# Kernel optimization log

Hardware: AMD Instinct MI355X
Metric: run time of the kernel (lower is better)

## Reference

```python
import jax, jax.numpy as jnp
import numpy as np

B, N, D = 1, 40962, 512
H, HD = 4, 128            # num_heads, key_size=value_size=d_model//num_heads
BS = 256                  # mask_block_size
NB = 161                  # num blocks = ceil(N/BS)
NP = NB * BS              # padded nodes = 41216
PAD = NP - N              # num_padding_nodes = 254
C = 16                    # global_norm_conditioning dim
FFW = 4 * D
SCALE = HD ** -0.5


def _build_mask():
    valid = (np.arange(NP) < N).reshape(NB, BS)            # key validity per block
    md = np.broadcast_to(valid[:, None, :], (NB, BS, BS))  # diag: keys of block n
    mu = np.zeros((NB, BS, BS), bool)
    mu[:-1] = np.broadcast_to(valid[1:, None, :], (NB - 1, BS, BS))   # upper: block n+1
    ml = np.zeros((NB, BS, BS), bool)
    ml[1:] = np.broadcast_to(valid[:-1, None, :], (NB - 1, BS, BS))   # lower: block n-1
    m = np.stack([md, mu, ml])[None, :, :, None]           # [1,3,NB,1,BS,BS]
    return jnp.asarray(m)


def setup_inputs() -> dict:
    key = jax.random.key(0)
    ks = jax.random.split(key, 12)
    s = 0.02
    return {
        'x': jax.random.normal(ks[0], (B, N, D), jnp.float32),
        'global_norm_conditioning': jax.random.normal(ks[1], (B, C), jnp.float32),
        'mask': _build_mask(),
        'wq': jax.random.normal(ks[2], (D, H * HD), jnp.float32) * s,
        'wk': jax.random.normal(ks[3], (D, H * HD), jnp.float32) * s,
        'wv': jax.random.normal(ks[4], (D, H * HD), jnp.float32) * s,
        'w_final': jax.random.normal(ks[5], (H * HD, D), jnp.float32) * s,
        'b_final': jnp.zeros((D,), jnp.float32),
        'w_up': jax.random.normal(ks[6], (D, FFW), jnp.float32) * s,
        'b_up': jnp.zeros((FFW,), jnp.float32),
        'w_down': jax.random.normal(ks[7], (FFW, D), jnp.float32) * s,
        'b_down': jnp.zeros((D,), jnp.float32),
        'w_cond': jax.random.normal(ks[8], (C, 2 * D), jnp.float32) * s,
        'b_cond': jnp.zeros((2 * D,), jnp.float32),
    }


def _layernorm(h):
    mu = h.mean(-1, keepdims=True)
    var = h.var(-1, keepdims=True)
    return (h - mu) * jax.lax.rsqrt(var + 1e-5)


def _triblock_attn(h, mask, wq, wk, wv, w_final, b_final):
    hp = jnp.pad(h, ((0, 0), (0, PAD), (0, 0))).reshape(B, NB, BS, D)
    q = (hp @ wq).reshape(B, NB, BS, H, HD)
    k = (hp @ wk).reshape(B, NB, BS, H, HD)
    v = (hp @ wv).reshape(B, NB, BS, H, HD)
    k = jnp.pad(k, ((0, 0), (1, 1), (0, 0), (0, 0), (0, 0)))
    v = jnp.pad(v, ((0, 0), (1, 1), (0, 0), (0, 0), (0, 0)))
    qk = lambda kk: jnp.einsum('bnqhd,bnkhd->bnhqk', q, kk) * SCALE
    ld = jnp.where(mask[:, 0], qk(k[:, 1:-1]), -1e30)
    lu = jnp.where(mask[:, 1], qk(k[:, 2:]), -1e30)
    ll = jnp.where(mask[:, 2], qk(k[:, :-2]), -1e30)
    # tri-block softmax with shared max/denominator
    m = jnp.maximum(jnp.maximum(
        jax.lax.stop_gradient(ld.max(-1, keepdims=True)),
        jax.lax.stop_gradient(lu.max(-1, keepdims=True))),
        jax.lax.stop_gradient(ll.max(-1, keepdims=True)))
    ed, eu, el = jnp.exp(ld - m), jnp.exp(lu - m), jnp.exp(ll - m)
    denom = ed.sum(-1, keepdims=True) + eu.sum(-1, keepdims=True) + el.sum(-1, keepdims=True)
    av = lambda w, vv: jnp.einsum('bnhqk,bnkhd->bnqhd', w, vv)
    o = av(ed / denom, v[:, 1:-1]) + av(eu / denom, v[:, 2:]) + av(el / denom, v[:, :-2])
    o = o.reshape(B, NP, H * HD) @ w_final + b_final
    return o[:, :N, :]


def reference(x, global_norm_conditioning, mask, wq, wk, wv, w_final, b_final,
              w_up, b_up, w_down, b_down, w_cond, b_cond):
    so = global_norm_conditioning @ w_cond + b_cond       # [B, 2D]
    scale, offset = jnp.split(so[:, None, :], 2, axis=-1)  # [B,1,D] each
    cond = lambda h: h * (scale + 1.0) + offset
    x = x + _triblock_attn(cond(_layernorm(x)), mask, wq, wk, wv, w_final, b_final)
    h = cond(_layernorm(x))
    x = x + (jax.nn.gelu(h @ w_up + b_up) @ w_down + b_down)
    return x
```

## Files before the change

### kernel.cpp

```cpp
#include <hip/hip_runtime.h>
#include <stdint.h>
#include <stddef.h>

#define NNODES 40962
#define NBLK   161
#define NP     41216
#define DM     512
#define NH     4
#define HD     128
#define SCALE_ATT 0.08838834764831845f

typedef __attribute__((ext_vector_type(8))) short short8;
typedef __attribute__((ext_vector_type(4))) float f32x4;
typedef __attribute__((ext_vector_type(4))) unsigned short us4;
typedef __attribute__((ext_vector_type(8))) __bf16 bf16x8;

__device__ __forceinline__ unsigned short f2bf(float f){
  unsigned u = __builtin_bit_cast(unsigned, f);
  u += 0x7fffu + ((u >> 16) & 1u);
  return (unsigned short)(u >> 16);
}
__device__ __forceinline__ float bf2f(unsigned short h){
  unsigned u = ((unsigned)h) << 16;
  return __builtin_bit_cast(float, u);
}
__device__ __forceinline__ unsigned char f2fp8(float f){
  return (unsigned char)(__builtin_amdgcn_cvt_pk_fp8_f32(f, 0.f, 0, false) & 0xff);
}
__device__ __forceinline__ float gelu_tanh(float x){
  float y = 0.7978845608028654f * (x + 0.044715f * x * x * x);
  y = fminf(fmaxf(y, -15.f), 15.f);
  float t = __expf(2.f * y);
  return x * t / (t + 1.f);
}
__device__ __forceinline__ bf16x8 ldb8(const unsigned short* p){
  return *(const bf16x8*)p;
}
#define MFMA(a,b,c) __builtin_amdgcn_mfma_f32_16x16x32_bf16((a),(b),(c),0,0,0)
#define MFMA8(a,b,c) __builtin_amdgcn_mfma_f32_16x16x32_fp8_fp8((a),(b),(c),0,0,0)

#define GLOAD16(g, l) \
  __builtin_amdgcn_global_load_lds((const __attribute__((address_space(1))) unsigned int*)(g), \
                                   (__attribute__((address_space(3))) unsigned int*)(l), 16, 0, 0)

__global__ void k_cond(const float* __restrict__ gnc, const float* __restrict__ wc,
                       const float* __restrict__ bc, float* __restrict__ cond){
  int j = blockIdx.x * 256 + threadIdx.x;
  float acc = bc[j];
  #pragma unroll
  for(int c = 0; c < 16; ++c) acc += gnc[c] * wc[c * 1024 + j];
  cond[j] = (j < 512) ? acc + 1.0f : acc;
}

__global__ __launch_bounds__(256) void k_transpose_f8(const float* __restrict__ W,
                                                      unsigned char* __restrict__ Wt,
                                                      int K, int Ncols){
  __shared__ float tile[32][33];
  int n0 = blockIdx.x * 32, k0 = blockIdx.y * 32;
  int tx = threadIdx.x & 31, ty = threadIdx.x >> 5;
  #pragma unroll
  for(int i = 0; i < 4; ++i){
    int r = ty + i * 8;
    tile[r][tx] = W[(size_t)(k0 + r) * Ncols + n0 + tx];
  }
  __syncthreads();
  #pragma unroll
  for(int i = 0; i < 4; ++i){
    int r = ty + i * 8;
    Wt[(size_t)(n0 + r) * K + k0 + tx] = f2fp8(tile[tx][r]);
  }
}

__global__ __launch_bounds__(256) void k_lncond(const void* __restrict__ xin, int in_bf16,
                                                const float* __restrict__ cond,
                                                void* __restrict__ outv, int out_f8,
                                                int Mvalid){
  int lane = threadIdx.x & 63;
  int row = blockIdx.x * 4 + (threadIdx.x >> 6);
  if(row >= Mvalid){
    if(out_f8){
      unsigned char* orow = (unsigned char*)outv + (size_t)row * DM + lane * 8;
      *(uint2*)orow = make_uint2(0, 0);
    } else {
      unsigned short* orow = (unsigned short*)outv + (size_t)row * DM + lane * 8;
      *(uint4*)orow = make_uint4(0,0,0,0);
    }
    return;
  }
  float v[8];
  if(in_bf16){
    const unsigned short* xr = (const unsigned short*)xin + (size_t)row * DM + lane * 8;
    us4 a = *(const us4*)xr, b = *(const us4*)(xr + 4);
    #pragma unroll
    for(int j = 0; j < 4; ++j){ v[j] = bf2f(a[j]); v[4+j] = bf2f(b[j]); }
  } else {
    const float* xr = (const float*)xin + (size_t)row * DM + lane * 8;
    float4 a = *(const float4*)xr;
    float4 b = *(const float4*)(xr + 4);
    v[0]=a.x; v[1]=a.y; v[2]=a.z; v[3]=a.w; v[4]=b.x; v[5]=b.y; v[6]=b.z; v[7]=b.w;
  }
  float s = 0.f, s2 = 0.f;
  #pragma unroll
  for(int j = 0; j < 8; ++j){ s += v[j]; s2 += v[j]*v[j]; }
  #pragma unroll
  for(int off = 1; off < 64; off <<= 1){ s += __shfl_xor(s, off); s2 += __shfl_xor(s2, off); }
  float mu = s * (1.f/DM);
  float var = s2 * (1.f/DM) - mu*mu;
  float rs = rsqrtf(var + 1e-5f);
  float scv[8], ofv[8];
  {
    float4 sc0 = *(const float4*)(cond + lane*8);
    float4 sc1 = *(const float4*)(cond + lane*8 + 4);
    float4 of0 = *(const float4*)(cond + 512 + lane*8);
    float4 of1 = *(const float4*)(cond + 512 + lane*8 + 4);
    scv[0]=sc0.x;scv[1]=sc0.y;scv[2]=sc0.z;scv[3]=sc0.w;
    scv[4]=sc1.x;scv[5]=sc1.y;scv[6]=sc1.z;scv[7]=sc1.w;
    ofv[0]=of0.x;ofv[1]=of0.y;ofv[2]=of0.z;ofv[3]=of0.w;
    ofv[4]=of1.x;ofv[5]=of1.y;ofv[6]=of1.z;ofv[7]=of1.w;
  }
  float o8[8];
  #pragma unroll
  for(int j = 0; j < 8; ++j) o8[j] = (v[j] - mu) * rs * scv[j] + ofv[j];
  if(out_f8){
    unsigned char* orow = (unsigned char*)outv + (size_t)row * DM + lane * 8;
    unsigned lo = 0, hi = 0;
    #pragma unroll
    for(int j = 0; j < 4; ++j) lo |= ((unsigned)f2fp8(o8[j])) << (8*j);
    #pragma unroll
    for(int j = 0; j < 4; ++j) hi |= ((unsigned)f2fp8(o8[4+j])) << (8*j);
    *(uint2*)orow = make_uint2(lo, hi);
  } else {
    unsigned short* orow = (unsigned short*)outv + (size_t)row * DM + lane * 8;
    unsigned pk[4];
    #pragma unroll
    for(int j = 0; j < 4; ++j)
      pk[j] = (unsigned)f2bf(o8[2*j]) | ((unsigned)f2bf(o8[2*j+1]) << 16);
    *(uint4*)orow = make_uint4(pk[0],pk[1],pk[2],pk[3]);
  }
}

#define GF_GELU   1
#define GF_RESF32 4
#define GF_QKV    8
#define GF_F8OUT  16

__global__ __launch_bounds__(256, 3)
void k_g128_f8(const unsigned char* __restrict__ A, int lda,
               const unsigned char* __restrict__ Bt, int ldb,
               const float* __restrict__ bias,
               const void* __restrict__ resid, int ldr,
               void* __restrict__ out, int ldo,
               void* __restrict__ out_k, void* __restrict__ out_vt,
               int Mstore, int NT, int Nblks, int flags)
{
  __shared__ __align__(16) unsigned char As[128*128];
  __shared__ __align__(16) unsigned char Bs[128*128];
  const int tid = threadIdx.x;
  const int lane = tid & 63, l15 = lane & 15, lg = lane >> 4;
  const int w = tid >> 6, wm = w >> 1, wn = w & 1;
  int nwg = gridDim.x;
  int q = nwg >> 3, r = nwg & 7;
  int xcd = blockIdx.x & 7, idx = blockIdx.x >> 3;
  int sid = (xcd < r ? xcd * (q + 1) : r * (q + 1) + (xcd - r) * q) + idx;
  int mblk = sid / Nblks, nblk = sid % Nblks;
  const int m0 = mblk * 128, n0 = nblk * 128;

  int srow[4], scol[4];
  #pragma unroll
  for(int rr = 0; rr < 4; ++rr){
    unsigned L = (unsigned)rr * 4096u + (unsigned)tid * 16u;
    unsigned sw = L ^ (((L >> 7) & 7u) << 4);
    srow[rr] = sw >> 7;
    scol[rr] = sw & 127u;
  }
  const unsigned wbase = (unsigned)w * 1024u;

  f32x4 acc[4][4];
  #pragma unroll
  for(int i = 0; i < 4; ++i)
    #pragma unroll
    for(int j = 0; j < 4; ++j) acc[i][j] = (f32x4)0.0f;

  for(int ks = 0; ks < NT; ++ks){
    #pragma unroll
    for(int rr = 0; rr < 4; ++rr)
      GLOAD16(A + (size_t)(m0 + srow[rr]) * lda + ks*128 + scol[rr],
              (char*)As + rr*4096 + wbase);
    #pragma unroll
    for(int rr = 0; rr < 4; ++rr)
      GLOAD16(Bt + (size_t)(n0 + srow[rr]) * ldb + ks*128 + scol[rr],
              (char*)Bs + rr*4096 + wbase);
    __syncthreads();
    #pragma unroll
    for(int kk = 0; kk < 4; ++kk){
      const unsigned csw = (unsigned)((kk*32 + lg*8) ^ ((l15 & 7) << 4));
      long la[4], lb[4];
      #pragma unroll
      for(int mi = 0; mi < 4; ++mi)
        la[mi] = *(const long*)(As + (wm*64 + mi*16 + l15)*128 + csw);
      #pragma unroll
      for(int ni = 0; ni < 4; ++ni)
        lb[ni] = *(const long*)(Bs + (wn*64 + ni*16 + l15)*128 + csw);
      #pragma unroll
      for(int mi = 0; mi < 4; ++mi)
        #pragma unroll
        for(int ni = 0; ni < 4; ++ni)
          acc[mi][ni] = MFMA8(la[mi], lb[ni], acc[mi][ni]);
    }
    __syncthreads();
  }

  unsigned short* bdst = (unsigned short*)out;
  int cadj = 0;
  bool vtrans = false;
  bool qscale = false;
  if(flags & GF_QKV){
    if(n0 < 512)       { bdst = (unsigned short*)out;    cadj = 0; qscale = true; }
    else if(n0 < 1024) { bdst = (unsigned short*)out_k;  cadj = 512; }
    else               { bdst = (unsigned short*)out_vt; cadj = 1024; vtrans = true; }
  }
  #pragma unroll
  for(int mi = 0; mi < 4; ++mi){
    int rowb = m0 + wm*64 + mi*16 + lg*4;
    #pragma unroll
    for(int ni = 0; ni < 4; ++ni){
      int col = n0 + wn*64 + ni*16 + l15;
      float bc = bias ? bias[col] : 0.f;
      float vv[4];
      #pragma unroll
      for(int rr = 0; rr < 4; ++rr){
        float tt = acc[mi][ni][rr] + bc;
        if(flags & GF_GELU) tt = gelu_tanh(tt);
        if(qscale) tt *= SCALE_ATT;
        vv[rr] = tt;
      }
      if(flags & GF_QKV){
        if(vtrans){
          us4 pk;
          #pragma unroll
          for(int rr = 0; rr < 4; ++rr) pk[rr] = f2bf(vv[rr]);
          *(us4*)(bdst + (size_t)(col - cadj)*NP + rowb) = pk;
        } else {
          #pragma unroll
          for(int rr = 0; rr < 4; ++rr)
            bdst[(size_t)(rowb + rr)*ldo + col - cadj] = f2bf(vv[rr]);
        }
      } else if(flags & GF_F8OUT){
        #pragma unroll
        for(int rr = 0; rr < 4; ++rr)
          ((unsigned char*)out)[(size_t)(rowb + rr)*ldo + col] = f2fp8(vv[rr]);
      } else if(flags & GF_RESF32){
        #pragma unroll
        for(int rr = 0; rr < 4; ++rr){
          int row = rowb + rr;
          if(row < Mstore){
            float tt = vv[rr] + ((const float*)resid)[(size_t)row*ldr + col];
            ((unsigned short*)out)[(size_t)row*ldo + col] = f2bf(tt);
          }
        }
      } else {
        #pragma unroll
        for(int rr = 0; rr < 4; ++rr){
          int row = rowb + rr;
          if(row < Mstore){
            float tt = vv[rr]
                     + bf2f(((const unsigned short*)resid)[(size_t)row*ldr + col]);
            ((float*)out)[(size_t)row*ldo + col] = tt;
          }
        }
      }
    }
  }
}

__global__ __launch_bounds__(512, 4)
void k_attn(const unsigned short* __restrict__ q_g, const unsigned short* __restrict__ k_g,
            const unsigned short* __restrict__ vt_g, unsigned char* __restrict__ o_g8)
{
  __shared__ __align__(16) unsigned short kv[128*128];
  __shared__ __align__(16) unsigned short p_lds[8*16*136];
  int b = blockIdx.x;
  int g = (b & 7) * 161 + (b >> 3);
  int n = g >> 3, rg = (g >> 2) & 1, h = g & 3;
  int tid = threadIdx.x;
  int w = tid >> 6, lane = tid & 63, l15 = lane & 15, lg = lane >> 4;
  int qbase = n*256 + rg*128 + w*16;
  unsigned short* pw = p_lds + w*16*136;
  const int rsw = (l15 & 7) << 3;
  const int srow = tid >> 4, scs = (tid & 15) * 8;

  bf16x8 aq[4];
  {
    const unsigned short* qp = q_g + (size_t)(qbase + l15)*DM + h*HD + lg*8;
    #pragma unroll
    for(int kb = 0; kb < 4; ++kb) aq[kb] = ldb8(qp + kb*32);
  }
  f32x4 oacc[8];
  #pragma unroll
  for(int t = 0; t < 8; ++t) oacc[t] = (f32x4)0.0f;
  float denom[4] = {0.f,0.f,0.f,0.f};

  #define COORDS(j, K0, VCH) do {                                    \
    int d_ = (j) >> 1, ch_ = (j) & 1;                                \
    int nb_ = n + (d_ == 1 ? 1 : (d_ == 2 ? -1 : 0));                \
    int nbc_ = nb_ < 0 ? 0 : (nb_ >= NBLK ? NBLK - 1 : nb_);         \
    (K0) = nbc_*256 + ch_*128;                                       \
    (VCH) = (nb_ >= 0) && (nb_ < NBLK) && ((K0) < NNODES);           \
  } while(0)

  short8 kreg[4], vreg[4];
  int k0; bool vch;
  COORDS(0, k0, vch);
  #pragma unroll
  for(int i = 0; i < 4; ++i){
    int row = srow + i*32;
    kreg[i] = *(const short8*)(k_g + (size_t)(k0+row)*DM + h*HD + scs);
    vreg[i] = *(const short8*)(vt_g + (size_t)(h*HD+row)*NP + k0 + scs);
  }

  #pragma unroll 1
  for(int j = 0; j < 6; ++j){
    int k0n = 0; bool vchn = false;
    const bool hn = (j < 5);
    if(hn) COORDS(j+1, k0n, vchn);
    __syncthreads();
    #pragma unroll
    for(int i = 0; i < 4; ++i){
      int row = srow + i*32;
      *(short8*)(kv + row*128 + (scs ^ ((row & 7) << 3))) = kreg[i];
    }
    __syncthreads();
    if(hn){
      #pragma unroll
      for(int i = 0; i < 4; ++i){
        int row = srow + i*32;
        kreg[i] = *(const short8*)(k_g + (size_t)(k0n+row)*DM + h*HD + scs);
      }
    }
    float rsum[4] = {0.f,0.f,0.f,0.f};
    #pragma unroll
    for(int t = 0; t < 8; ++t){
      f32x4 s = (f32x4)0.0f;
      #pragma unroll
      for(int kb = 0; kb < 4; ++kb){
        bf16x8 bk = ldb8(kv + (t*16 + l15)*128 + ((kb*32 + lg*8) ^ rsw));
        s = MFMA(aq[kb], bk, s);
      }
      bool kval = vch && ((k0 + t*16 + l15) < NNODES);
      #pragma unroll
      for(int r = 0; r < 4; ++r){
        float p = kval ? __expf(s[r]) : 0.f;
        rsum[r] += p;
        pw[(lg*4 + r)*136 + t*16 + l15] = f2bf(p);
      }
    }
    #pragma unroll
    for(int r = 0; r < 4; ++r){
      float s_ = rsum[r];
      s_ += __shfl_xor(s_, 1); s_ += __shfl_xor(s_, 2);
      s_ += __shfl_xor(s_, 4); s_ += __shfl_xor(s_, 8);
      denom[r] += s_;
    }
    __syncthreads();
    #pragma unroll
    for(int i = 0; i < 4; ++i){
      int row = srow + i*32;
      *(short8*)(kv + row*128 + (scs ^ ((row & 7) << 3))) = vreg[i];
    }
    __syncthreads();
    if(hn){
      #pragma unroll
      for(int i = 0; i < 4; ++i){
        int row = srow + i*32;
        vreg[i] = *(const short8*)(vt_g + (size_t)(h*HD+row)*NP + k0n + scs);
      }
    }
    __builtin_amdgcn_s_setprio(1);
    #pragma unroll
    for(int kb2 = 0; kb2 < 4; ++kb2){
      bf16x8 ap = ldb8(pw + l15*136 + kb2*32 + lg*8);
      #pragma unroll
      for(int t2 = 0; t2 < 8; ++t2){
        bf16x8 bv = ldb8(kv + (t2*16 + l15)*128 + ((kb2*32 + lg*8) ^ rsw));
        oacc[t2] = MFMA(ap, bv, oacc[t2]);
      }
    }
    __builtin_amdgcn_s_setprio(0);
    k0 = k0n; vch = vchn;
  }
  float inv[4];
  #pragma unroll
  for(int r = 0; r < 4; ++r) inv[r] = 1.0f / denom[r];
  #pragma unroll
  for(int t2 = 0; t2 < 8; ++t2){
    #pragma unroll
    for(int r = 0; r < 4; ++r){
      o_g8[(size_t)(qbase + lg*4 + r)*DM + h*HD + t2*16 + l15] =
        f2fp8(oacc[t2][r] * inv[r]);
    }
  }
}

extern "C" void kernel_launch(void* const* d_in, const int* in_sizes, int n_in,
                              void* d_out, int out_size, void* d_ws, size_t ws_size,
                              hipStream_t stream)
{
  const float* x    = (const float*)d_in[0];
  const float* gnc  = (const float*)d_in[1];
  const float* wq   = (const float*)d_in[3];
  const float* wk   = (const float*)d_in[4];
  const float* wv   = (const float*)d_in[5];
  const float* wf   = (const float*)d_in[6];
  const float* bfin = (const float*)d_in[7];
  const float* wup  = (const float*)d_in[8];
  const float* bup  = (const float*)d_in[9];
  const float* wdn  = (const float*)d_in[10];
  const float* bdn  = (const float*)d_in[11];
  const float* wc   = (const float*)d_in[12];
  const float* bc   = (const float*)d_in[13];
  float* out = (float*)d_out;

  char* ws = (char*)d_ws;
  size_t off = 0;
  auto alloc = [&](size_t bytes)->void*{
    void* p = ws + off;
    off += (bytes + 255) & ~(size_t)255;
    return p;
  };
  float*          cond    = (float*)alloc(1024u*4);
  unsigned char*  wqkv_f8 = (unsigned char*)alloc((size_t)1536*512);
  unsigned char*  wf_f8   = (unsigned char*)alloc((size_t)512*512);
  unsigned char*  wup_f8  = (unsigned char*)alloc((size_t)2048*512);
  unsigned char*  wdn_f8  = (unsigned char*)alloc((size_t)512*2048);
  unsigned char*  hp8     = (unsigned char*)alloc((size_t)NP*DM);
  unsigned short* kbuf    = (unsigned short*)alloc((size_t)NP*DM*2);
  unsigned short* vtbuf   = (unsigned short*)alloc((size_t)NP*DM*2);
  unsigned short* qbuf    = (unsigned short*)alloc((size_t)NP*DM*2);
  unsigned char*  obuf8   = (unsigned char*)alloc((size_t)NP*DM);
  unsigned short* x1      = (unsigned short*)alloc((size_t)NP*DM*2);
  unsigned char*  ubuf8   = (unsigned char*)alloc((size_t)NP*2048);
  (void)ws_size; (void)in_sizes; (void)n_in; (void)out_size;

  k_cond<<<4, 256, 0, stream>>>(gnc, wc, bc, cond);
  k_transpose_f8<<<dim3(16,16), 256, 0, stream>>>(wq, wqkv_f8,            512, 512);
  k_transpose_f8<<<dim3(16,16), 256, 0, stream>>>(wk, wqkv_f8 + 512*512,  512, 512);
  k_transpose_f8<<<dim3(16,16), 256, 0, stream>>>(wv, wqkv_f8 + 1024*512, 512, 512);
  k_transpose_f8<<<dim3(16,16), 256, 0, stream>>>(wf, wf_f8,  512, 512);
  k_transpose_f8<<<dim3(64,16), 256, 0, stream>>>(wup, wup_f8, 512, 2048);
  k_transpose_f8<<<dim3(16,64), 256, 0, stream>>>(wdn, wdn_f8, 2048, 512);
  k_lncond<<<NP/4, 256, 0, stream>>>(x, 0, cond, hp8, 1, NNODES);
  k_g128_f8<<<322*12, 256, 0, stream>>>(hp8, 512, wqkv_f8, 512, nullptr, nullptr, 0,
                                        qbuf, 512, kbuf, vtbuf, NP, 4, 12, GF_QKV);
  k_attn<<<1288, 512, 0, stream>>>(qbuf, kbuf, vtbuf, obuf8);
  k_g128_f8<<<322*4, 256, 0, stream>>>(obuf8, 512, wf_f8, 512, bfin, x, 512,
                                       x1, 512, nullptr, nullptr, NNODES, 4, 4,
                                       GF_RESF32);
  k_lncond<<<NP/4, 256, 0, stream>>>(x1, 1, cond, hp8, 1, NNODES);
  k_g128_f8<<<322*16, 256, 0, stream>>>(hp8, 512, wup_f8, 512, bup, nullptr, 0,
                                        ubuf8, 2048, nullptr, nullptr, NP, 4, 16,
                                        GF_GELU | GF_F8OUT);
  k_g128_f8<<<322*4, 256, 0, stream>>>(ubuf8, 2048, wdn_f8, 2048, bdn, x1, 512,
                                       out, 512, nullptr, nullptr, NNODES, 16, 4, 0);
}
```

Baseline: 557.1 us.

## Store Q/K/V in FP8 and run attention MFMAs in FP8

The QKV GEMM epilogue now writes Q, K and transposed V as FP8 bytes instead of bf16. The attention kernel loads FP8 operands and uses 16x16x32 fp8 MFMAs for both QK^T and PV, quantizing the probabilities to FP8 as well. The softmax scale moves from the Q store to the exp argument. This halves Q/K/V memory traffic and LDS footprint, at the cost of reduced accuracy in the scores and the probability-weighted sums.

```diff
diff --git a/kernel.cpp b/kernel.cpp
--- a/kernel.cpp
+++ b/kernel.cpp
@@ -13,6 +13,7 @@
 typedef __attribute__((ext_vector_type(8))) short short8;
 typedef __attribute__((ext_vector_type(4))) float f32x4;
 typedef __attribute__((ext_vector_type(4))) unsigned short us4;
+typedef __attribute__((ext_vector_type(2))) unsigned long long u64x2;
 typedef __attribute__((ext_vector_type(8))) __bf16 bf16x8;
 
 __device__ __forceinline__ unsigned short f2bf(float f){
@@ -36,7 +37,6 @@
 __device__ __forceinline__ bf16x8 ldb8(const unsigned short* p){
   return *(const bf16x8*)p;
 }
-#define MFMA(a,b,c) __builtin_amdgcn_mfma_f32_16x16x32_bf16((a),(b),(c),0,0,0)
 #define MFMA8(a,b,c) __builtin_amdgcn_mfma_f32_16x16x32_fp8_fp8((a),(b),(c),0,0,0)
 
 #define GLOAD16(g, l) \
@@ -210,15 +210,6 @@
     __syncthreads();
   }
 
-  unsigned short* bdst = (unsigned short*)out;
-  int cadj = 0;
-  bool vtrans = false;
-  bool qscale = false;
-  if(flags & GF_QKV){
-    if(n0 < 512)       { bdst = (unsigned short*)out;    cadj = 0; qscale = true; }
-    else if(n0 < 1024) { bdst = (unsigned short*)out_k;  cadj = 512; }
-    else               { bdst = (unsigned short*)out_vt; cadj = 1024; vtrans = true; }
-  }
   #pragma unroll
   for(int mi = 0; mi < 4; ++mi){
     int rowb = m0 + wm*64 + mi*16 + lg*4;
@@ -231,19 +222,22 @@
       for(int rr = 0; rr < 4; ++rr){
         float tt = acc[mi][ni][rr] + bc;
         if(flags & GF_GELU) tt = gelu_tanh(tt);
-        if(qscale) tt *= SCALE_ATT;
         vv[rr] = tt;
       }
       if(flags & GF_QKV){
-        if(vtrans){
-          us4 pk;
-          #pragma unroll
-          for(int rr = 0; rr < 4; ++rr) pk[rr] = f2bf(vv[rr]);
-          *(us4*)(bdst + (size_t)(col - cadj)*NP + rowb) = pk;
-        } else {
+        if(n0 < 512){
           #pragma unroll
           for(int rr = 0; rr < 4; ++rr)
-            bdst[(size_t)(rowb + rr)*ldo + col - cadj] = f2bf(vv[rr]);
+            ((unsigned char*)out)[(size_t)(rowb + rr)*ldo + col] = f2fp8(vv[rr]);
+        } else if(n0 < 1024){
+          #pragma unroll
+          for(int rr = 0; rr < 4; ++rr)
+            ((unsigned char*)out_k)[(size_t)(rowb + rr)*ldo + col - 512] = f2fp8(vv[rr]);
+        } else {
+          unsigned pk = 0;
+          #pragma unroll
+          for(int rr = 0; rr < 4; ++rr) pk |= ((unsigned)f2fp8(vv[rr])) << (8*rr);
+          *(unsigned*)((unsigned char*)out_vt + (size_t)(col - 1024)*NP + rowb) = pk;
         }
       } else if(flags & GF_F8OUT){
         #pragma unroll
@@ -274,26 +268,26 @@
 }
 
 __global__ __launch_bounds__(512, 4)
-void k_attn(const unsigned short* __restrict__ q_g, const unsigned short* __restrict__ k_g,
-            const unsigned short* __restrict__ vt_g, unsigned char* __restrict__ o_g8)
+void k_attn(const unsigned char* __restrict__ q_g, const unsigned char* __restrict__ k_g,
+            const unsigned char* __restrict__ vt_g, unsigned char* __restrict__ o_g8)
 {
-  __shared__ __align__(16) unsigned short kv[128*128];
-  __shared__ __align__(16) unsigned short p_lds[8*16*136];
+  __shared__ __align__(16) unsigned char kv[128*128];
+  __shared__ __align__(16) unsigned char p_lds[8*16*136];
   int b = blockIdx.x;
   int g = (b & 7) * 161 + (b >> 3);
   int n = g >> 3, rg = (g >> 2) & 1, h = g & 3;
   int tid = threadIdx.x;
   int w = tid >> 6, lane = tid & 63, l15 = lane & 15, lg = lane >> 4;
   int qbase = n*256 + rg*128 + w*16;
-  unsigned short* pw = p_lds + w*16*136;
+  unsigned char* pw = p_lds + w*16*136;
   const int rsw = (l15 & 7) << 3;
-  const int srow = tid >> 4, scs = (tid & 15) * 8;
-
-  bf16x8 aq[4];
+  const int srow = tid >> 3, scs = (tid & 7) * 16;
+
+  long aq[4];
   {
-    const unsigned short* qp = q_g + (size_t)(qbase + l15)*DM + h*HD + lg*8;
-    #pragma unroll
-    for(int kb = 0; kb < 4; ++kb) aq[kb] = ldb8(qp + kb*32);
+    const unsigned char* qp = q_g + (size_t)(qbase + l15)*DM + h*HD;
+    #pragma unroll
+    for(int kb = 0; kb < 4; ++kb) aq[kb] = *(const long*)(qp + kb*32 + lg*8);
   }
   f32x4 oacc[8];
   #pragma unroll
@@ -308,14 +302,14 @@
     (VCH) = (nb_ >= 0) && (nb_ < NBLK) && ((K0) < NNODES);           \
   } while(0)
 
-  short8 kreg[4], vreg[4];
+  u64x2 kreg[2], vreg[2];
   int k0; bool vch;
   COORDS(0, k0, vch);
   #pragma unroll
-  for(int i = 0; i < 4; ++i){
-    int row = srow + i*32;
-    kreg[i] = *(const short8*)(k_g + (size_t)(k0+row)*DM + h*HD + scs);
-    vreg[i] = *(const short8*)(vt_g + (size_t)(h*HD+row)*NP + k0 + scs);
+  for(int i = 0; i < 2; ++i){
+    int row = srow + i*64;
+    kreg[i] = *(const u64x2*)(k_g + (size_t)(k0+row)*DM + h*HD + scs);
+    vreg[i] = *(const u64x2*)(vt_g + (size_t)(h*HD+row)*NP + k0 + scs);
   }
 
   #pragma unroll 1
@@ -325,16 +319,18 @@
     if(hn) COORDS(j+1, k0n, vchn);
     __syncthreads();
     #pragma unroll
-    for(int i = 0; i < 4; ++i){
-      int row = srow + i*32;
-      *(short8*)(kv + row*128 + (scs ^ ((row & 7) << 3))) = kreg[i];
+    for(int i = 0; i < 2; ++i){
+      int row = srow + i*64;
+      int base = row*128, sz = (row & 7) << 3;
+      *(unsigned long long*)(kv + base + ((scs    ) ^ sz)) = kreg[i][0];
+      *(unsigned long long*)(kv + base + ((scs + 8) ^ sz)) = kreg[i][1];
     }
     __syncthreads();
     if(hn){
       #pragma unroll
-      for(int i = 0; i < 4; ++i){
-        int row = srow + i*32;
-        kreg[i] = *(const short8*)(k_g + (size_t)(k0n+row)*DM + h*HD + scs);
+      for(int i = 0; i < 2; ++i){
+        int row = srow + i*64;
+        kreg[i] = *(const u64x2*)(k_g + (size_t)(k0n+row)*DM + h*HD + scs);
       }
     }
     float rsum[4] = {0.f,0.f,0.f,0.f};
@@ -343,15 +339,15 @@
       f32x4 s = (f32x4)0.0f;
       #pragma unroll
       for(int kb = 0; kb < 4; ++kb){
-        bf16x8 bk = ldb8(kv + (t*16 + l15)*128 + ((kb*32 + lg*8) ^ rsw));
-        s = MFMA(aq[kb], bk, s);
+        long bk = *(const long*)(kv + (t*16 + l15)*128 + ((kb*32 + lg*8) ^ rsw));
+        s = MFMA8(aq[kb], bk, s);
       }
       bool kval = vch && ((k0 + t*16 + l15) < NNODES);
       #pragma unroll
       for(int r = 0; r < 4; ++r){
-        float p = kval ? __expf(s[r]) : 0.f;
+        float p = kval ? __expf(s[r] * SCALE_ATT) : 0.f;
         rsum[r] += p;
-        pw[(lg*4 + r)*136 + t*16 + l15] = f2bf(p);
+        pw[(lg*4 + r)*136 + t*16 + l15] = f2fp8(p);
       }
     }
     #pragma unroll
@@ -363,26 +359,28 @@
     }
     __syncthreads();
     #pragma unroll
-    for(int i = 0; i < 4; ++i){
-      int row = srow + i*32;
-      *(short8*)(kv + row*128 + (scs ^ ((row & 7) << 3))) = vreg[i];
+    for(int i = 0; i < 2; ++i){
+      int row = srow + i*64;
+      int base = row*128, sz = (row & 7) << 3;
+      *(unsigned long long*)(kv + base + ((scs    ) ^ sz)) = vreg[i][0];
+      *(unsigned long long*)(kv + base + ((scs + 8) ^ sz)) = vreg[i][1];
     }
     __syncthreads();
     if(hn){
       #pragma unroll
-      for(int i = 0; i < 4; ++i){
-        int row = srow + i*32;
-        vreg[i] = *(const short8*)(vt_g + (size_t)(h*HD+row)*NP + k0n + scs);
+      for(int i = 0; i < 2; ++i){
+        int row = srow + i*64;
+        vreg[i] = *(const u64x2*)(vt_g + (size_t)(h*HD+row)*NP + k0n + scs);
       }
     }
     __builtin_amdgcn_s_setprio(1);
     #pragma unroll
     for(int kb2 = 0; kb2 < 4; ++kb2){
-      bf16x8 ap = ldb8(pw + l15*136 + kb2*32 + lg*8);
+      long ap = *(const long*)(pw + l15*136 + kb2*32 + lg*8);
       #pragma unroll
       for(int t2 = 0; t2 < 8; ++t2){
-        bf16x8 bv = ldb8(kv + (t2*16 + l15)*128 + ((kb2*32 + lg*8) ^ rsw));
-        oacc[t2] = MFMA(ap, bv, oacc[t2]);
+        long bv = *(const long*)(kv + (t2*16 + l15)*128 + ((kb2*32 + lg*8) ^ rsw));
+        oacc[t2] = MFMA8(ap, bv, oacc[t2]);
       }
     }
     __builtin_amdgcn_s_setprio(0);
@@ -433,9 +431,9 @@
   unsigned char*  wup_f8  = (unsigned char*)alloc((size_t)2048*512);
   unsigned char*  wdn_f8  = (unsigned char*)alloc((size_t)512*2048);
   unsigned char*  hp8     = (unsigned char*)alloc((size_t)NP*DM);
-  unsigned short* kbuf    = (unsigned short*)alloc((size_t)NP*DM*2);
-  unsigned short* vtbuf   = (unsigned short*)alloc((size_t)NP*DM*2);
-  unsigned short* qbuf    = (unsigned short*)alloc((size_t)NP*DM*2);
+  unsigned char*  kbuf8   = (unsigned char*)alloc((size_t)NP*DM);
+  unsigned char*  vtbuf8  = (unsigned char*)alloc((size_t)NP*DM);
+  unsigned char*  qbuf8   = (unsigned char*)alloc((size_t)NP*DM);
   unsigned char*  obuf8   = (unsigned char*)alloc((size_t)NP*DM);
   unsigned short* x1      = (unsigned short*)alloc((size_t)NP*DM*2);
   unsigned char*  ubuf8   = (unsigned char*)alloc((size_t)NP*2048);
@@ -450,8 +448,8 @@
   k_transpose_f8<<<dim3(16,64), 256, 0, stream>>>(wdn, wdn_f8, 2048, 512);
   k_lncond<<<NP/4, 256, 0, stream>>>(x, 0, cond, hp8, 1, NNODES);
   k_g128_f8<<<322*12, 256, 0, stream>>>(hp8, 512, wqkv_f8, 512, nullptr, nullptr, 0,
-                                        qbuf, 512, kbuf, vtbuf, NP, 4, 12, GF_QKV);
-  k_attn<<<1288, 512, 0, stream>>>(qbuf, kbuf, vtbuf, obuf8);
+                                        qbuf8, 512, kbuf8, vtbuf8, NP, 4, 12, GF_QKV);
+  k_attn<<<1288, 512, 0, stream>>>(qbuf8, kbuf8, vtbuf8, obuf8);
   k_g128_f8<<<322*4, 256, 0, stream>>>(obuf8, 512, wf_f8, 512, bfin, x, 512,
                                        x1, 512, nullptr, nullptr, NNODES, 4, 4,
                                        GF_RESF32);
```

Result: faster. 533.2 us (-4.3%).
